# Performance work log

Hardware: AMD Instinct MI355X
Metric: run time of the kernel (lower is better)

The kernel has to match this reference:

```python
import jax, jax.numpy as jnp
import numpy as np

B, T, D, R, V = 8, 512, 1024, 4, 2048


def setup_inputs() -> dict:
    key = jax.random.key(0)
    k1, k2, k3, k4, k5 = jax.random.split(key, 5)
    return {
        "input_embs": jax.random.normal(k1, (B, T, D), dtype=jnp.float32),
        "label_ids": jax.random.randint(k2, (B, T), 0, V),
        "w_alpha": jax.random.normal(k3, (D, R), dtype=jnp.float32),
        "w_beta": jax.random.normal(k4, (D, R), dtype=jnp.float32),
        "w_vocab": jax.random.normal(k5, (D, V * R * R), dtype=jnp.float32),
    }


def _normalize(m, axis):
    # torch normalize_matrix: abs then divide by sum over `dim` (rows of the matrix)
    m = jnp.abs(m)
    return m / m.sum(axis=axis, keepdims=True)


def reference(input_embs, label_ids, w_alpha, w_beta, w_vocab):
    x = input_embs
    Bq, Tq, Dq = x.shape
    xf = x.reshape(-1, Dq)                                   # [B*T, D]
    alpha = (xf @ w_alpha).reshape(Bq, Tq, R).mean(1)        # [B, R]
    beta = (xf @ w_beta).reshape(Bq, Tq, R).mean(1)          # [B, R]
    core = (xf @ w_vocab).reshape(Bq, Tq, R, V, R).mean(1)   # [B, R, V, R]

    # gather core slices core[b, :, y[b,k], :] -> [B, T, R, R]
    g = jnp.take_along_axis(core.transpose(0, 2, 1, 3),      # [B, V, R, R]
                            label_ids[:, :, None, None], axis=1)
    Mn = _normalize(g, axis=2)                               # normalize over matrix rows (dim=0)

    v = _normalize(alpha, axis=1)                            # [B, R] normalized column vector
    Ms = Mn.transpose(1, 0, 2, 3)                            # [T, B, R, R]

    def step(v, M):
        return jnp.einsum('bij,bj->bi', M, v), None

    v, _ = jax.lax.scan(step, v, Ms)                         # sequential TT chain over T
    nb = _normalize(beta, axis=1)                            # [B, R]
    probs = jnp.einsum('bi,bi->b', nb, v)                    # [B]
    loss = -jnp.log(probs)
    return loss.mean()
```

## Files before the change

kernel.cpp:

```cpp
#include <hip/hip_runtime.h>
#include <math.h>

#define Bq 8
#define T 512
#define D 1024
#define R 4
#define V 2048
#define NCOL (V * R * R)
#define DSPLIT 16
#define DCHUNK (D / DSPLIT)
#define CBLK 1024
#define NTC 32

__global__ void k_xbar(const float* __restrict__ x, float* __restrict__ partial,
                       float* __restrict__ out) {
    int b   = blockIdx.x;
    int tc  = blockIdx.y;
    int tid = threadIdx.x;
    if (b == 0 && tc == 0 && tid == 0) out[0] = 0.f;
    const float4* xp = (const float4*)(x + ((size_t)b * T + (size_t)tc * 16) * D) + tid;
    float4 acc = make_float4(0.f, 0.f, 0.f, 0.f);
#pragma unroll
    for (int t = 0; t < 16; ++t) {
        float4 v = xp[t * (D / 4)];
        acc.x += v.x; acc.y += v.y; acc.z += v.z; acc.w += v.w;
    }
    *(float4*)(partial + ((size_t)b * NTC + tc) * D + tid * 4) = acc;
}

__global__ void k_core(const float* __restrict__ wv, const float* __restrict__ partial,
                       float* __restrict__ xbar, float* __restrict__ part) {
    __shared__ float xs[Bq * DCHUNK];
    int tid  = threadIdx.x;
    int colb = blockIdx.x;
    int ds   = blockIdx.y;
    int d0   = ds * DCHUNK;

#pragma unroll
    for (int h = 0; h < 2; ++h) {
        int q  = tid + h * 256;
        int b  = q >> 6;
        int dd = q & 63;
        const float* pp = partial + (size_t)b * NTC * D + d0 + dd;
        float s = 0.f;
#pragma unroll
        for (int tc = 0; tc < NTC; ++tc) s += pp[(size_t)tc * D];
        xs[q] = s;
    }
    __syncthreads();

    if (colb == 0 && tid < 128) {
        int q4 = tid * 4;
        int b  = q4 >> 6;
        int dd = q4 & 63;
        *(float4*)(xbar + b * D + d0 + dd) = *(const float4*)(xs + q4);
    }

    int col = colb * CBLK + tid * 4;
    const float4* wp = (const float4*)(wv + (size_t)d0 * NCOL + col);
    float4 acc[Bq];
#pragma unroll
    for (int b = 0; b < Bq; ++b) acc[b] = make_float4(0.f, 0.f, 0.f, 0.f);

#pragma unroll 8
    for (int d = 0; d < DCHUNK; ++d) {
        float4 w = wp[(size_t)d * (NCOL / 4)];
#pragma unroll
        for (int b = 0; b < Bq; ++b) {
            float xv = xs[b * DCHUNK + d];
            acc[b].x += w.x * xv;
            acc[b].y += w.y * xv;
            acc[b].z += w.z * xv;
            acc[b].w += w.w * xv;
        }
    }

#pragma unroll
    for (int b = 0; b < Bq; ++b)
        *(float4*)(part + ((size_t)ds * Bq + b) * NCOL + col) = acc[b];
}

__global__ void k_gather(const float* __restrict__ part, const int* __restrict__ labels,
                         float* __restrict__ bprod) {
    __shared__ float Mn_s[64 * 16];
    __shared__ float gm[8][17];
    int b   = blockIdx.x;
    int tc  = blockIdx.y;
    int tid = threadIdx.x;
    int tl  = tid >> 2;
    int i   = tid & 3;
    int t   = tc * 64 + tl;
    int y   = labels[b * T + t];

    const float* pb = part + (size_t)b * NCOL + (size_t)i * (V * R) + (size_t)y * R;
    float4 g = make_float4(0.f, 0.f, 0.f, 0.f);
#pragma unroll
    for (int ds = 0; ds < DSPLIT; ++ds) {
        float4 v = *(const float4*)(pb + (size_t)ds * (Bq * NCOL));
        g.x += v.x; g.y += v.y; g.z += v.z; g.w += v.w;
    }
    g.x = fabsf(g.x); g.y = fabsf(g.y); g.z = fabsf(g.z); g.w = fabsf(g.w);

    float sx = g.x, sy = g.y, sz = g.z, sw = g.w;
    sx += __shfl_xor(sx, 1); sy += __shfl_xor(sy, 1);
    sz += __shfl_xor(sz, 1); sw += __shfl_xor(sw, 1);
    sx += __shfl_xor(sx, 2); sy += __shfl_xor(sy, 2);
    sz += __shfl_xor(sz, 2); sw += __shfl_xor(sw, 2);

    float4 o = make_float4(g.x / sx, g.y / sy, g.z / sz, g.w / sw);
    *(float4*)(Mn_s + tl * 16 + i * 4) = o;
    __syncthreads();

    int c = tid;
    if (c < 8) {
        const float* mp = Mn_s + c * 8 * 16;
        float P[R][R];
        {
            float4 m0 = *(const float4*)(mp + 0);
            float4 m1 = *(const float4*)(mp + 4);
            float4 m2 = *(const float4*)(mp + 8);
            float4 m3 = *(const float4*)(mp + 12);
            P[0][0]=m0.x; P[0][1]=m0.y; P[0][2]=m0.z; P[0][3]=m0.w;
            P[1][0]=m1.x; P[1][1]=m1.y; P[1][2]=m1.z; P[1][3]=m1.w;
            P[2][0]=m2.x; P[2][1]=m2.y; P[2][2]=m2.z; P[2][3]=m2.w;
            P[3][0]=m3.x; P[3][1]=m3.y; P[3][2]=m3.z; P[3][3]=m3.w;
        }
#pragma unroll
        for (int k = 1; k < 8; ++k) {
            float4 m0 = *(const float4*)(mp + k * 16 + 0);
            float4 m1 = *(const float4*)(mp + k * 16 + 4);
            float4 m2 = *(const float4*)(mp + k * 16 + 8);
            float4 m3 = *(const float4*)(mp + k * 16 + 12);
            float M[R][R] = {{m0.x, m0.y, m0.z, m0.w},
                             {m1.x, m1.y, m1.z, m1.w},
                             {m2.x, m2.y, m2.z, m2.w},
                             {m3.x, m3.y, m3.z, m3.w}};
            float N[R][R];
#pragma unroll
            for (int ii = 0; ii < R; ++ii)
#pragma unroll
                for (int j = 0; j < R; ++j)
                    N[ii][j] = M[ii][0] * P[0][j] + M[ii][1] * P[1][j] +
                               M[ii][2] * P[2][j] + M[ii][3] * P[3][j];
#pragma unroll
            for (int ii = 0; ii < R; ++ii)
#pragma unroll
                for (int j = 0; j < R; ++j) P[ii][j] = N[ii][j];
        }
#pragma unroll
        for (int ii = 0; ii < R; ++ii)
#pragma unroll
            for (int j = 0; j < R; ++j) gm[c][ii * 4 + j] = P[ii][j];
    }
    __syncthreads();

    for (int rnd = 0; rnd < 3; ++rnd) {
        int step = 1 << rnd;
        bool act = (c < 8) && ((c & (2 * step - 1)) == 0);
        float N2[R][R];
        if (act) {
            float A[R][R], Bm[R][R];
#pragma unroll
            for (int ii = 0; ii < R; ++ii)
#pragma unroll
                for (int j = 0; j < R; ++j) {
                    A[ii][j]  = gm[c + step][ii * 4 + j];
                    Bm[ii][j] = gm[c][ii * 4 + j];
                }
#pragma unroll
            for (int ii = 0; ii < R; ++ii)
#pragma unroll
                for (int j = 0; j < R; ++j)
                    N2[ii][j] = A[ii][0] * Bm[0][j] + A[ii][1] * Bm[1][j] +
                                A[ii][2] * Bm[2][j] + A[ii][3] * Bm[3][j];
        }
        __syncthreads();
        if (act) {
#pragma unroll
            for (int ii = 0; ii < R; ++ii)
#pragma unroll
                for (int j = 0; j < R; ++j) gm[c][ii * 4 + j] = N2[ii][j];
        }
        __syncthreads();
    }

    if (tid < 4)
        *(float4*)(bprod + ((size_t)(b * 8 + tc)) * 16 + tid * 4) =
            *(const float4*)(&gm[0][tid * 4]);
}

__global__ void k_chain(const float* __restrict__ bprod, const float* __restrict__ xbar,
                        const float* __restrict__ wa, const float* __restrict__ wb,
                        float* __restrict__ out) {
    __shared__ float mats[8][17];
    __shared__ float abp[64];
    int b   = blockIdx.x;
    int tid = threadIdx.x;

    {
        int r   = tid & 3;
        int sel = (tid >> 2) & 1;
        int seg = tid >> 3;
        const float* w  = sel ? wb : wa;
        const float* xp = xbar + b * D;
        float s = 0.f;
#pragma unroll 8
        for (int d = seg * 128; d < seg * 128 + 128; ++d)
            s += xp[d] * w[d * R + r];
        abp[tid] = s;
    }

    if (tid < 32) {
        int c = tid >> 2, q = tid & 3;
        *(float4*)(&mats[c][q * 4]) =
            *(const float4*)(bprod + ((size_t)(b * 8 + c)) * 16 + q * 4);
    }
    __syncthreads();

    int c = tid;
    for (int rnd = 0; rnd < 3; ++rnd) {
        int step = 1 << rnd;
        bool act = (c < 8) && ((c & (2 * step - 1)) == 0);
        float N2[R][R];
        if (act) {
            float A[R][R], Bm[R][R];
#pragma unroll
            for (int i = 0; i < R; ++i)
#pragma unroll
                for (int j = 0; j < R; ++j) {
                    A[i][j]  = mats[c + step][i * 4 + j];
                    Bm[i][j] = mats[c][i * 4 + j];
                }
#pragma unroll
            for (int i = 0; i < R; ++i)
#pragma unroll
                for (int j = 0; j < R; ++j)
                    N2[i][j] = A[i][0] * Bm[0][j] + A[i][1] * Bm[1][j] +
                               A[i][2] * Bm[2][j] + A[i][3] * Bm[3][j];
        }
        __syncthreads();
        if (act) {
#pragma unroll
            for (int i = 0; i < R; ++i)
#pragma unroll
                for (int j = 0; j < R; ++j) mats[c][i * 4 + j] = N2[i][j];
        }
        __syncthreads();
    }

    if (tid == 0) {
        float a[R], be[R];
#pragma unroll
        for (int r = 0; r < R; ++r) {
            float sa = 0.f, sb = 0.f;
#pragma unroll
            for (int seg = 0; seg < 8; ++seg) {
                sa += abp[(seg << 3) | r];
                sb += abp[(seg << 3) | 4 | r];
            }
            a[r] = sa; be[r] = sb;
        }
        float sa = fabsf(a[0]) + fabsf(a[1]) + fabsf(a[2]) + fabsf(a[3]);
        float v0[R];
#pragma unroll
        for (int r = 0; r < R; ++r) v0[r] = fabsf(a[r]) / sa;
        float v[R];
#pragma unroll
        for (int i = 0; i < R; ++i)
            v[i] = mats[0][i * 4 + 0] * v0[0] + mats[0][i * 4 + 1] * v0[1] +
                   mats[0][i * 4 + 2] * v0[2] + mats[0][i * 4 + 3] * v0[3];
        float sb = fabsf(be[0]) + fabsf(be[1]) + fabsf(be[2]) + fabsf(be[3]);
        float prob = (fabsf(be[0]) * v[0] + fabsf(be[1]) * v[1] +
                      fabsf(be[2]) * v[2] + fabsf(be[3]) * v[3]) / sb;
        atomicAdd(out, -logf(prob) * 0.125f);
    }
}

extern "C" void kernel_launch(void* const* d_in, const int* in_sizes, int n_in,
                              void* d_out, int out_size, void* d_ws, size_t ws_size,
                              hipStream_t stream) {
    const float* x      = (const float*)d_in[0];
    const int*   labels = (const int*)d_in[1];
    const float* wa     = (const float*)d_in[2];
    const float* wb     = (const float*)d_in[3];
    const float* wv     = (const float*)d_in[4];
    float* out = (float*)d_out;

    float* xbar    = (float*)d_ws;
    float* partial = xbar + Bq * D;
    float* part    = partial + (size_t)Bq * NTC * D;
    float* bprod   = part + (size_t)DSPLIT * Bq * NCOL;

    k_xbar<<<dim3(Bq, NTC), 256, 0, stream>>>(x, partial, out);
    k_core<<<dim3(NCOL / CBLK, DSPLIT), 256, 0, stream>>>(wv, partial, xbar, part);
    k_gather<<<dim3(Bq, 8), 256, 0, stream>>>(part, labels, bprod);
    k_chain<<<Bq, 64, 0, stream>>>(bprod, xbar, wa, wb, out);
}
```

Before: 232.8 us.

## Fuse four kernels into one cooperative kernel with grid-wide syncs

Replaces the four separate launches (x mean, core projection, gather/normalize/chain, final reduction) with a single cooperative kernel of 512 blocks that separates the phases with grid.sync(). The xbar reduction becomes its own phase run by 32 blocks instead of being recomputed redundantly by every core block. This is meant to cut the gaps between launches and the per-launch overhead. In exchange it adds four grid-wide barriers and leaves most blocks idle during the small phases.

```diff
diff --git a/kernel.cpp b/kernel.cpp
--- a/kernel.cpp
+++ b/kernel.cpp
@@ -1,5 +1,8 @@
 #include <hip/hip_runtime.h>
+#include <hip/hip_cooperative_groups.h>
 #include <math.h>
+
+namespace cg = cooperative_groups;
 
 #define Bq 8
 #define T 512
@@ -11,268 +14,276 @@
 #define DCHUNK (D / DSPLIT)
 #define CBLK 1024
 #define NTC 32
-
-__global__ void k_xbar(const float* __restrict__ x, float* __restrict__ partial,
-                       float* __restrict__ out) {
-    int b   = blockIdx.x;
-    int tc  = blockIdx.y;
-    int tid = threadIdx.x;
-    if (b == 0 && tc == 0 && tid == 0) out[0] = 0.f;
-    const float4* xp = (const float4*)(x + ((size_t)b * T + (size_t)tc * 16) * D) + tid;
-    float4 acc = make_float4(0.f, 0.f, 0.f, 0.f);
-#pragma unroll
-    for (int t = 0; t < 16; ++t) {
-        float4 v = xp[t * (D / 4)];
-        acc.x += v.x; acc.y += v.y; acc.z += v.z; acc.w += v.w;
-    }
-    *(float4*)(partial + ((size_t)b * NTC + tc) * D + tid * 4) = acc;
-}
-
-__global__ void k_core(const float* __restrict__ wv, const float* __restrict__ partial,
-                       float* __restrict__ xbar, float* __restrict__ part) {
+#define NBLK 512
+
+__global__ __launch_bounds__(256, 2)
+void k_fused(const float* __restrict__ x, const int* __restrict__ labels,
+             const float* __restrict__ wa, const float* __restrict__ wb,
+             const float* __restrict__ wv, float* __restrict__ out,
+             float* __restrict__ partial, float* __restrict__ xbar,
+             float* __restrict__ part, float* __restrict__ bprod)
+{
+    cg::grid_group grid = cg::this_grid();
+    const int bid = blockIdx.x;
+    const int tid = threadIdx.x;
+
     __shared__ float xs[Bq * DCHUNK];
-    int tid  = threadIdx.x;
-    int colb = blockIdx.x;
-    int ds   = blockIdx.y;
-    int d0   = ds * DCHUNK;
-
-#pragma unroll
-    for (int h = 0; h < 2; ++h) {
-        int q  = tid + h * 256;
-        int b  = q >> 6;
-        int dd = q & 63;
-        const float* pp = partial + (size_t)b * NTC * D + d0 + dd;
-        float s = 0.f;
-#pragma unroll
-        for (int tc = 0; tc < NTC; ++tc) s += pp[(size_t)tc * D];
-        xs[q] = s;
-    }
-    __syncthreads();
-
-    if (colb == 0 && tid < 128) {
-        int q4 = tid * 4;
-        int b  = q4 >> 6;
-        int dd = q4 & 63;
-        *(float4*)(xbar + b * D + d0 + dd) = *(const float4*)(xs + q4);
-    }
-
-    int col = colb * CBLK + tid * 4;
-    const float4* wp = (const float4*)(wv + (size_t)d0 * NCOL + col);
-    float4 acc[Bq];
-#pragma unroll
-    for (int b = 0; b < Bq; ++b) acc[b] = make_float4(0.f, 0.f, 0.f, 0.f);
-
-#pragma unroll 8
-    for (int d = 0; d < DCHUNK; ++d) {
-        float4 w = wp[(size_t)d * (NCOL / 4)];
-#pragma unroll
-        for (int b = 0; b < Bq; ++b) {
-            float xv = xs[b * DCHUNK + d];
-            acc[b].x += w.x * xv;
-            acc[b].y += w.y * xv;
-            acc[b].z += w.z * xv;
-            acc[b].w += w.w * xv;
-        }
-    }
-
-#pragma unroll
-    for (int b = 0; b < Bq; ++b)
-        *(float4*)(part + ((size_t)ds * Bq + b) * NCOL + col) = acc[b];
-}
-
-__global__ void k_gather(const float* __restrict__ part, const int* __restrict__ labels,
-                         float* __restrict__ bprod) {
     __shared__ float Mn_s[64 * 16];
     __shared__ float gm[8][17];
-    int b   = blockIdx.x;
-    int tc  = blockIdx.y;
-    int tid = threadIdx.x;
-    int tl  = tid >> 2;
-    int i   = tid & 3;
-    int t   = tc * 64 + tl;
-    int y   = labels[b * T + t];
-
-    const float* pb = part + (size_t)b * NCOL + (size_t)i * (V * R) + (size_t)y * R;
-    float4 g = make_float4(0.f, 0.f, 0.f, 0.f);
-#pragma unroll
-    for (int ds = 0; ds < DSPLIT; ++ds) {
-        float4 v = *(const float4*)(pb + (size_t)ds * (Bq * NCOL));
-        g.x += v.x; g.y += v.y; g.z += v.z; g.w += v.w;
-    }
-    g.x = fabsf(g.x); g.y = fabsf(g.y); g.z = fabsf(g.z); g.w = fabsf(g.w);
-
-    float sx = g.x, sy = g.y, sz = g.z, sw = g.w;
-    sx += __shfl_xor(sx, 1); sy += __shfl_xor(sy, 1);
-    sz += __shfl_xor(sz, 1); sw += __shfl_xor(sw, 1);
-    sx += __shfl_xor(sx, 2); sy += __shfl_xor(sy, 2);
-    sz += __shfl_xor(sz, 2); sw += __shfl_xor(sw, 2);
-
-    float4 o = make_float4(g.x / sx, g.y / sy, g.z / sz, g.w / sw);
-    *(float4*)(Mn_s + tl * 16 + i * 4) = o;
-    __syncthreads();
-
-    int c = tid;
-    if (c < 8) {
-        const float* mp = Mn_s + c * 8 * 16;
-        float P[R][R];
-        {
-            float4 m0 = *(const float4*)(mp + 0);
-            float4 m1 = *(const float4*)(mp + 4);
-            float4 m2 = *(const float4*)(mp + 8);
-            float4 m3 = *(const float4*)(mp + 12);
-            P[0][0]=m0.x; P[0][1]=m0.y; P[0][2]=m0.z; P[0][3]=m0.w;
-            P[1][0]=m1.x; P[1][1]=m1.y; P[1][2]=m1.z; P[1][3]=m1.w;
-            P[2][0]=m2.x; P[2][1]=m2.y; P[2][2]=m2.z; P[2][3]=m2.w;
-            P[3][0]=m3.x; P[3][1]=m3.y; P[3][2]=m3.z; P[3][3]=m3.w;
-        }
-#pragma unroll
-        for (int k = 1; k < 8; ++k) {
-            float4 m0 = *(const float4*)(mp + k * 16 + 0);
-            float4 m1 = *(const float4*)(mp + k * 16 + 4);
-            float4 m2 = *(const float4*)(mp + k * 16 + 8);
-            float4 m3 = *(const float4*)(mp + k * 16 + 12);
-            float M[R][R] = {{m0.x, m0.y, m0.z, m0.w},
-                             {m1.x, m1.y, m1.z, m1.w},
-                             {m2.x, m2.y, m2.z, m2.w},
-                             {m3.x, m3.y, m3.z, m3.w}};
-            float N[R][R];
+    __shared__ float abp[64];
+
+    if (bid < 256) {
+        int b  = bid >> 5;
+        int tc = bid & 31;
+        if (bid == 0 && tid == 0) out[0] = 0.f;
+        const float4* xp = (const float4*)(x + ((size_t)b * T + (size_t)tc * 16) * D) + tid;
+        float4 acc = make_float4(0.f, 0.f, 0.f, 0.f);
+#pragma unroll
+        for (int t = 0; t < 16; ++t) {
+            float4 v = xp[t * (D / 4)];
+            acc.x += v.x; acc.y += v.y; acc.z += v.z; acc.w += v.w;
+        }
+        *(float4*)(partial + ((size_t)b * NTC + tc) * D + tid * 4) = acc;
+    }
+    grid.sync();
+
+    if (bid < 32) {
+        int q  = bid * 256 + tid;
+        int b  = q >> 10;
+        int dd = q & 1023;
+        const float* pp = partial + (size_t)b * NTC * D + dd;
+        float s = 0.f;
+#pragma unroll
+        for (int tc = 0; tc < NTC; ++tc) s += pp[(size_t)tc * D];
+        xbar[q] = s;
+    }
+    grid.sync();
+
+    {
+        int colb = bid & 31;
+        int ds   = bid >> 5;
+        int d0   = ds * DCHUNK;
+
+#pragma unroll
+        for (int h = 0; h < 2; ++h) {
+            int q  = tid + h * 256;
+            int b  = q >> 6;
+            int dd = q & 63;
+            xs[q] = xbar[b * D + d0 + dd];
+        }
+        __syncthreads();
+
+        int col = colb * CBLK + tid * 4;
+        const float4* wp = (const float4*)(wv + (size_t)d0 * NCOL + col);
+        float4 acc[Bq];
+#pragma unroll
+        for (int b = 0; b < Bq; ++b) acc[b] = make_float4(0.f, 0.f, 0.f, 0.f);
+
+#pragma unroll 8
+        for (int d = 0; d < DCHUNK; ++d) {
+            float4 w = wp[(size_t)d * (NCOL / 4)];
+#pragma unroll
+            for (int b = 0; b < Bq; ++b) {
+                float xv = xs[b * DCHUNK + d];
+                acc[b].x += w.x * xv;
+                acc[b].y += w.y * xv;
+                acc[b].z += w.z * xv;
+                acc[b].w += w.w * xv;
+            }
+        }
+
+#pragma unroll
+        for (int b = 0; b < Bq; ++b)
+            *(float4*)(part + ((size_t)ds * Bq + b) * NCOL + col) = acc[b];
+    }
+    grid.sync();
+
+    if (bid < 64) {
+        int b   = bid >> 3;
+        int tc  = bid & 7;
+        int tl  = tid >> 2;
+        int i   = tid & 3;
+        int t   = tc * 64 + tl;
+        int y   = labels[b * T + t];
+
+        const float* pb = part + (size_t)b * NCOL + (size_t)i * (V * R) + (size_t)y * R;
+        float4 g = make_float4(0.f, 0.f, 0.f, 0.f);
+#pragma unroll
+        for (int ds = 0; ds < DSPLIT; ++ds) {
+            float4 v = *(const float4*)(pb + (size_t)ds * (Bq * NCOL));
+            g.x += v.x; g.y += v.y; g.z += v.z; g.w += v.w;
+        }
+        g.x = fabsf(g.x); g.y = fabsf(g.y); g.z = fabsf(g.z); g.w = fabsf(g.w);
+
+        float sx = g.x, sy = g.y, sz = g.z, sw = g.w;
+        sx += __shfl_xor(sx, 1); sy += __shfl_xor(sy, 1);
+        sz += __shfl_xor(sz, 1); sw += __shfl_xor(sw, 1);
+        sx += __shfl_xor(sx, 2); sy += __shfl_xor(sy, 2);
+        sz += __shfl_xor(sz, 2); sw += __shfl_xor(sw, 2);
+
+        float4 o = make_float4(g.x / sx, g.y / sy, g.z / sz, g.w / sw);
+        *(float4*)(Mn_s + tl * 16 + i * 4) = o;
+        __syncthreads();
+
+        int c = tid;
+        if (c < 8) {
+            const float* mp = Mn_s + c * 8 * 16;
+            float P[R][R];
+            {
+                float4 m0 = *(const float4*)(mp + 0);
+                float4 m1 = *(const float4*)(mp + 4);
+                float4 m2 = *(const float4*)(mp + 8);
+                float4 m3 = *(const float4*)(mp + 12);
+                P[0][0]=m0.x; P[0][1]=m0.y; P[0][2]=m0.z; P[0][3]=m0.w;
+                P[1][0]=m1.x; P[1][1]=m1.y; P[1][2]=m1.z; P[1][3]=m1.w;
+                P[2][0]=m2.x; P[2][1]=m2.y; P[2][2]=m2.z; P[2][3]=m2.w;
+                P[3][0]=m3.x; P[3][1]=m3.y; P[3][2]=m3.z; P[3][3]=m3.w;
+            }
+#pragma unroll
+            for (int k = 1; k < 8; ++k) {
+                float4 m0 = *(const float4*)(mp + k * 16 + 0);
+                float4 m1 = *(const float4*)(mp + k * 16 + 4);
+                float4 m2 = *(const float4*)(mp + k * 16 + 8);
+                float4 m3 = *(const float4*)(mp + k * 16 + 12);
+                float M[R][R] = {{m0.x, m0.y, m0.z, m0.w},
+                                 {m1.x, m1.y, m1.z, m1.w},
+                                 {m2.x, m2.y, m2.z, m2.w},
+                                 {m3.x, m3.y, m3.z, m3.w}};
+                float N[R][R];
+#pragma unroll
+                for (int ii = 0; ii < R; ++ii)
+#pragma unroll
+                    for (int j = 0; j < R; ++j)
+                        N[ii][j] = M[ii][0] * P[0][j] + M[ii][1] * P[1][j] +
+                                   M[ii][2] * P[2][j] + M[ii][3] * P[3][j];
+#pragma unroll
+                for (int ii = 0; ii < R; ++ii)
+#pragma unroll
+                    for (int j = 0; j < R; ++j) P[ii][j] = N[ii][j];
+            }
 #pragma unroll
             for (int ii = 0; ii < R; ++ii)
 #pragma unroll
-                for (int j = 0; j < R; ++j)
-                    N[ii][j] = M[ii][0] * P[0][j] + M[ii][1] * P[1][j] +
-                               M[ii][2] * P[2][j] + M[ii][3] * P[3][j];
-#pragma unroll
-            for (int ii = 0; ii < R; ++ii)
-#pragma unroll
-                for (int j = 0; j < R; ++j) P[ii][j] = N[ii][j];
-        }
-#pragma unroll
-        for (int ii = 0; ii < R; ++ii)
-#pragma unroll
-            for (int j = 0; j < R; ++j) gm[c][ii * 4 + j] = P[ii][j];
-    }
-    __syncthreads();
-
-    for (int rnd = 0; rnd < 3; ++rnd) {
-        int step = 1 << rnd;
-        bool act = (c < 8) && ((c & (2 * step - 1)) == 0);
-        float N2[R][R];
-        if (act) {
-            float A[R][R], Bm[R][R];
-#pragma unroll
-            for (int ii = 0; ii < R; ++ii)
-#pragma unroll
-                for (int j = 0; j < R; ++j) {
-                    A[ii][j]  = gm[c + step][ii * 4 + j];
-                    Bm[ii][j] = gm[c][ii * 4 + j];
+                for (int j = 0; j < R; ++j) gm[c][ii * 4 + j] = P[ii][j];
+        }
+        __syncthreads();
+
+        for (int rnd = 0; rnd < 3; ++rnd) {
+            int step = 1 << rnd;
+            bool act = (c < 8) && ((c & (2 * step - 1)) == 0);
+            float N2[R][R];
+            if (act) {
+                float A[R][R], Bm[R][R];
+#pragma unroll
+                for (int ii = 0; ii < R; ++ii)
+#pragma unroll
+                    for (int j = 0; j < R; ++j) {
+                        A[ii][j]  = gm[c + step][ii * 4 + j];
+                        Bm[ii][j] = gm[c][ii * 4 + j];
+                    }
+#pragma unroll
+                for (int ii = 0; ii < R; ++ii)
+#pragma unroll
+                    for (int j = 0; j < R; ++j)
+                        N2[ii][j] = A[ii][0] * Bm[0][j] + A[ii][1] * Bm[1][j] +
+                                    A[ii][2] * Bm[2][j] + A[ii][3] * Bm[3][j];
+            }
+            __syncthreads();
+            if (act) {
+#pragma unroll
+                for (int ii = 0; ii < R; ++ii)
+#pragma unroll
+                    for (int j = 0; j < R; ++j) gm[c][ii * 4 + j] = N2[ii][j];
+            }
+            __syncthreads();
+        }
+
+        if (tid < 4)
+            *(float4*)(bprod + ((size_t)(b * 8 + tc)) * 16 + tid * 4) =
+                *(const float4*)(&gm[0][tid * 4]);
+    }
+    grid.sync();
+
+    if (bid < Bq) {
+        int b = bid;
+
+        if (tid < 64) {
+            int r   = tid & 3;
+            int sel = (tid >> 2) & 1;
+            int seg = tid >> 3;
+            const float* w  = sel ? wb : wa;
+            const float* xp = xbar + b * D;
+            float s = 0.f;
+#pragma unroll 8
+            for (int d = seg * 128; d < seg * 128 + 128; ++d)
+                s += xp[d] * w[d * R + r];
+            abp[tid] = s;
+        }
+
+        if (tid < 32) {
+            int c = tid >> 2, q = tid & 3;
+            *(float4*)(&gm[c][q * 4]) =
+                *(const float4*)(bprod + ((size_t)(b * 8 + c)) * 16 + q * 4);
+        }
+        __syncthreads();
+
+        int c = tid;
+        for (int rnd = 0; rnd < 3; ++rnd) {
+            int step = 1 << rnd;
+            bool act = (c < 8) && ((c & (2 * step - 1)) == 0);
+            float N2[R][R];
+            if (act) {
+                float A[R][R], Bm[R][R];
+#pragma unroll
+                for (int i = 0; i < R; ++i)
+#pragma unroll
+                    for (int j = 0; j < R; ++j) {
+                        A[i][j]  = gm[c + step][i * 4 + j];
+                        Bm[i][j] = gm[c][i * 4 + j];
+                    }
+#pragma unroll
+                for (int i = 0; i < R; ++i)
+#pragma unroll
+                    for (int j = 0; j < R; ++j)
+                        N2[i][j] = A[i][0] * Bm[0][j] + A[i][1] * Bm[1][j] +
+                                   A[i][2] * Bm[2][j] + A[i][3] * Bm[3][j];
+            }
+            __syncthreads();
+            if (act) {
+#pragma unroll
+                for (int i = 0; i < R; ++i)
+#pragma unroll
+                    for (int j = 0; j < R; ++j) gm[c][i * 4 + j] = N2[i][j];
+            }
+            __syncthreads();
+        }
+
+        if (tid == 0) {
+            float a[R], be[R];
+#pragma unroll
+            for (int r = 0; r < R; ++r) {
+                float sa = 0.f, sb = 0.f;
+#pragma unroll
+                for (int seg = 0; seg < 8; ++seg) {
+                    sa += abp[(seg << 3) | r];
+                    sb += abp[(seg << 3) | 4 | r];
                 }
-#pragma unroll
-            for (int ii = 0; ii < R; ++ii)
-#pragma unroll
-                for (int j = 0; j < R; ++j)
-                    N2[ii][j] = A[ii][0] * Bm[0][j] + A[ii][1] * Bm[1][j] +
-                                A[ii][2] * Bm[2][j] + A[ii][3] * Bm[3][j];
-        }
-        __syncthreads();
-        if (act) {
-#pragma unroll
-            for (int ii = 0; ii < R; ++ii)
-#pragma unroll
-                for (int j = 0; j < R; ++j) gm[c][ii * 4 + j] = N2[ii][j];
-        }
-        __syncthreads();
-    }
-
-    if (tid < 4)
-        *(float4*)(bprod + ((size_t)(b * 8 + tc)) * 16 + tid * 4) =
-            *(const float4*)(&gm[0][tid * 4]);
-}
-
-__global__ void k_chain(const float* __restrict__ bprod, const float* __restrict__ xbar,
-                        const float* __restrict__ wa, const float* __restrict__ wb,
-                        float* __restrict__ out) {
-    __shared__ float mats[8][17];
-    __shared__ float abp[64];
-    int b   = blockIdx.x;
-    int tid = threadIdx.x;
-
-    {
-        int r   = tid & 3;
-        int sel = (tid >> 2) & 1;
-        int seg = tid >> 3;
-        const float* w  = sel ? wb : wa;
-        const float* xp = xbar + b * D;
-        float s = 0.f;
-#pragma unroll 8
-        for (int d = seg * 128; d < seg * 128 + 128; ++d)
-            s += xp[d] * w[d * R + r];
-        abp[tid] = s;
-    }
-
-    if (tid < 32) {
-        int c = tid >> 2, q = tid & 3;
-        *(float4*)(&mats[c][q * 4]) =
-            *(const float4*)(bprod + ((size_t)(b * 8 + c)) * 16 + q * 4);
-    }
-    __syncthreads();
-
-    int c = tid;
-    for (int rnd = 0; rnd < 3; ++rnd) {
-        int step = 1 << rnd;
-        bool act = (c < 8) && ((c & (2 * step - 1)) == 0);
-        float N2[R][R];
-        if (act) {
-            float A[R][R], Bm[R][R];
+                a[r] = sa; be[r] = sb;
+            }
+            float sa = fabsf(a[0]) + fabsf(a[1]) + fabsf(a[2]) + fabsf(a[3]);
+            float v0[R];
+#pragma unroll
+            for (int r = 0; r < R; ++r) v0[r] = fabsf(a[r]) / sa;
+            float v[R];
 #pragma unroll
             for (int i = 0; i < R; ++i)
-#pragma unroll
-                for (int j = 0; j < R; ++j) {
-                    A[i][j]  = mats[c + step][i * 4 + j];
-                    Bm[i][j] = mats[c][i * 4 + j];
-                }
-#pragma unroll
-            for (int i = 0; i < R; ++i)
-#pragma unroll
-                for (int j = 0; j < R; ++j)
-                    N2[i][j] = A[i][0] * Bm[0][j] + A[i][1] * Bm[1][j] +
-                               A[i][2] * Bm[2][j] + A[i][3] * Bm[3][j];
-        }
-        __syncthreads();
-        if (act) {
-#pragma unroll
-            for (int i = 0; i < R; ++i)
-#pragma unroll
-                for (int j = 0; j < R; ++j) mats[c][i * 4 + j] = N2[i][j];
-        }
-        __syncthreads();
-    }
-
-    if (tid == 0) {
-        float a[R], be[R];
-#pragma unroll
-        for (int r = 0; r < R; ++r) {
-            float sa = 0.f, sb = 0.f;
-#pragma unroll
-            for (int seg = 0; seg < 8; ++seg) {
-                sa += abp[(seg << 3) | r];
-                sb += abp[(seg << 3) | 4 | r];
-            }
-            a[r] = sa; be[r] = sb;
-        }
-        float sa = fabsf(a[0]) + fabsf(a[1]) + fabsf(a[2]) + fabsf(a[3]);
-        float v0[R];
-#pragma unroll
-        for (int r = 0; r < R; ++r) v0[r] = fabsf(a[r]) / sa;
-        float v[R];
-#pragma unroll
-        for (int i = 0; i < R; ++i)
-            v[i] = mats[0][i * 4 + 0] * v0[0] + mats[0][i * 4 + 1] * v0[1] +
-                   mats[0][i * 4 + 2] * v0[2] + mats[0][i * 4 + 3] * v0[3];
-        float sb = fabsf(be[0]) + fabsf(be[1]) + fabsf(be[2]) + fabsf(be[3]);
-        float prob = (fabsf(be[0]) * v[0] + fabsf(be[1]) * v[1] +
-                      fabsf(be[2]) * v[2] + fabsf(be[3]) * v[3]) / sb;
-        atomicAdd(out, -logf(prob) * 0.125f);
+                v[i] = gm[0][i * 4 + 0] * v0[0] + gm[0][i * 4 + 1] * v0[1] +
+                       gm[0][i * 4 + 2] * v0[2] + gm[0][i * 4 + 3] * v0[3];
+            float sb = fabsf(be[0]) + fabsf(be[1]) + fabsf(be[2]) + fabsf(be[3]);
+            float prob = (fabsf(be[0]) * v[0] + fabsf(be[1]) * v[1] +
+                          fabsf(be[2]) * v[2] + fabsf(be[3]) * v[3]) / sb;
+            atomicAdd(out, -logf(prob) * 0.125f);
+        }
     }
 }
 
@@ -291,8 +302,9 @@
     float* part    = partial + (size_t)Bq * NTC * D;
     float* bprod   = part + (size_t)DSPLIT * Bq * NCOL;
 
-    k_xbar<<<dim3(Bq, NTC), 256, 0, stream>>>(x, partial, out);
-    k_core<<<dim3(NCOL / CBLK, DSPLIT), 256, 0, stream>>>(wv, partial, xbar, part);
-    k_gather<<<dim3(Bq, 8), 256, 0, stream>>>(part, labels, bprod);
-    k_chain<<<Bq, 64, 0, stream>>>(bprod, xbar, wa, wb, out);
+    void* args[] = {(void*)&x, (void*)&labels, (void*)&wa, (void*)&wb, (void*)&wv,
+                    (void*)&out, (void*)&partial, (void*)&xbar, (void*)&part,
+                    (void*)&bprod};
+    hipLaunchCooperativeKernel((const void*)k_fused, dim3(NBLK), dim3(256),
+                               args, 0, stream);
 }
```

Measured after the change: 461.1 us. 1.98x slower.
